# Optimization experiments

Hardware: AMD Instinct MI355X
Metric: run time of the kernel (lower is better)

Reference implementation:

```python
import jax, jax.numpy as jnp
import numpy as np

N, E, IN_DIM, HID = 50000, 800000, 128, 64
NEG_SLOPE = 0.01  # torch F.leaky_relu default


def setup_inputs() -> dict:
    key = jax.random.key(0)
    ks = jax.random.split(key, 8)
    x = jax.random.normal(ks[0], (N, IN_DIM), jnp.float32)
    edge_index = jax.random.randint(ks[1], (2, E), 0, N, dtype=jnp.int32)
    edge_weight = jax.random.uniform(ks[2], (E,), jnp.float32)
    h = jnp.zeros((N, HID), jnp.float32)
    c = jnp.zeros((N, HID), jnp.float32)
    sx = 1.0 / np.sqrt(IN_DIM)
    sh = 1.0 / np.sqrt(HID)
    # gate order along leading axis: [i, f, c(tilde), o]; K=2 Chebyshev weights
    Wx = (jax.random.normal(ks[3], (4, 2, IN_DIM, HID), jnp.float32) * sx)
    bx = jnp.zeros((4, HID), jnp.float32)
    Wh = (jax.random.normal(ks[4], (4, 2, HID, HID), jnp.float32) * sh)
    bh = jnp.zeros((4, HID), jnp.float32)
    wc = jax.random.normal(ks[5], (3, HID), jnp.float32) * 0.1  # peepholes for i, f, o
    bg = jnp.zeros((4, HID), jnp.float32)
    W_head = jax.random.normal(ks[6], (HID, 1), jnp.float32) * sh
    b_head = jnp.zeros((1,), jnp.float32)
    return dict(x=x, edge_index=edge_index, edge_weight=edge_weight, h=h, c=c,
                Wx=Wx, bx=bx, Wh=Wh, bh=bh, wc=wc, bg=bg, W_head=W_head, b_head=b_head)


def _cheb_norm(src, dst, ew, n):
    # ChebConv 'sym' normalization with lambda_max=2: L_hat = -D^{-1/2} A D^{-1/2}
    # (the +1 self-loop from the Laplacian cancels against fill_value=-1)
    deg = jnp.zeros((n,), ew.dtype).at[src].add(ew)
    dinv = jnp.where(deg > 0, 1.0 / jnp.sqrt(jnp.where(deg > 0, deg, 1.0)), 0.0)
    return -dinv[src] * ew * dinv[dst]


def _prop(feat, src, dst, norm, n):
    # T1 = L_hat @ feat via edge gather + segment-sum
    return jax.ops.segment_sum(norm[:, None] * feat[src], dst, num_segments=n)


def reference(x, edge_index, edge_weight, h, c, Wx, bx, Wh, bh, wc, bg, W_head, b_head):
    n = x.shape[0]
    src, dst = edge_index[0], edge_index[1]
    norm = _cheb_norm(src, dst, edge_weight, n)
    Tx = _prop(x, src, dst, norm, n)
    Th = _prop(h, src, dst, norm, n)  # shared across all 4 h-side ChebConvs
    # z[g] = X W[g,0] + (L_hat X) W[g,1] + b  for all gates at once
    z = (jnp.einsum('nd,gdh->gnh', x, Wx[:, 0]) + jnp.einsum('nd,gdh->gnh', Tx, Wx[:, 1]) + bx[:, None, :]
         + jnp.einsum('nd,gdh->gnh', h, Wh[:, 0]) + jnp.einsum('nd,gdh->gnh', Th, Wh[:, 1]) + bh[:, None, :])
    i = jax.nn.sigmoid(z[0] + wc[0] * c + bg[0])
    f = jax.nn.sigmoid(z[1] + wc[1] * c + bg[1])
    g = jnp.tanh(z[2] + bg[2])
    c_new = f * c + i * g
    o = jax.nn.sigmoid(z[3] + wc[2] * c_new + bg[3])
    h_new = o * jnp.tanh(c_new)
    out = jax.nn.leaky_relu(h_new, NEG_SLOPE) @ W_head + b_head
    return out, h_new, c_new
```

## Files before the change

### kernel.cpp

```cpp
#include <hip/hip_runtime.h>
#include <hip/hip_bf16.h>

#define IN_DIM 128
#define HID 64
#define NEG_SLOPE 0.01f
#define CAP 5120

typedef __attribute__((ext_vector_type(8))) short short8;
typedef __attribute__((ext_vector_type(4))) short short4v;
typedef __attribute__((ext_vector_type(4))) float f32x4;
typedef unsigned short ushort_t;
typedef unsigned int uint_t;

__device__ __forceinline__ float fsig(float x) { return 1.f / (1.f + __expf(-x)); }
__device__ __forceinline__ float ftanh(float x) { return 1.f - 2.f / (__expf(2.f * x) + 1.f); }

__device__ __forceinline__ ushort_t f2bf(float f) {
    uint_t u = __float_as_uint(f);
    uint_t r = u + 0x7fffu + ((u >> 16) & 1u);
    return (ushort_t)(r >> 16);
}
__device__ __forceinline__ float bf2f(ushort_t s) { return __uint_as_float(((uint_t)s) << 16); }
__device__ __forceinline__ float bf2f_s(short s) { return bf2f((ushort_t)s); }

__global__ __launch_bounds__(256) void cvt_kernel(
    const float* __restrict__ x, const float* __restrict__ h,
    const float* __restrict__ Wx, const float* __restrict__ Wh,
    uint_t* __restrict__ xb_u, uint_t* __restrict__ hb_u, ushort_t* __restrict__ Wp,
    int N) {
    int tid = blockIdx.x * 256 + threadIdx.x;
    int T = gridDim.x * 256;

    int ncvt = N * 96;
    int nx = N * 64;
    for (int i = tid; i < ncvt; i += T) {
        if (i < nx) {
            float2 v = ((const float2*)x)[i];
            xb_u[i] = (uint_t)f2bf(v.x) | ((uint_t)f2bf(v.y) << 16);
        } else {
            int j = i - nx;
            float2 v = ((const float2*)h)[j];
            hb_u[j] = (uint_t)f2bf(v.x) | ((uint_t)f2bf(v.y) << 16);
        }
    }

    for (int idx = tid; idx < 384 * 256; idx += T) {
        int j = idx & 7;
        int tmp = idx >> 3;
        int lane = tmp & 63;
        int t2 = tmp >> 6;
        int ct = t2 & 15;
        int ks = t2 >> 4;
        int k = ks * 32 + (lane >> 4) * 8 + j;
        int colg = ct * 16 + (lane & 15);
        int g = colg >> 6, hd = colg & 63;
        float v;
        if (k < 128)      v = Wx[((g * 2 + 0) * 128 + k) * 64 + hd];
        else if (k < 192) v = Wh[((g * 2 + 0) * 64 + (k - 128)) * 64 + hd];
        else if (k < 320) v = Wx[((g * 2 + 1) * 128 + (k - 192)) * 64 + hd];
        else              v = Wh[((g * 2 + 1) * 64 + (k - 320)) * 64 + hd];
        Wp[idx] = f2bf(v);
    }
}

__global__ __launch_bounds__(256) void part_kernel(
    const int* __restrict__ src, const int* __restrict__ dst, const float* __restrict__ ew,
    int* __restrict__ cur_d, int* __restrict__ cur_s,
    int2* __restrict__ dpart, int2* __restrict__ spart, int E) {
    __shared__ int hd[256], hs[256];
    int t = threadIdx.x;
    hd[t] = 0; hs[t] = 0;
    __syncthreads();
    int base = blockIdx.x * 2048;
    int sv[8], dv[8]; float wv[8];
#pragma unroll
    for (int it = 0; it < 8; ++it) {
        int e = base + it * 256 + t;
        bool ok = e < E;
        sv[it] = ok ? src[e] : 0;
        dv[it] = ok ? dst[e] : 0;
        wv[it] = ok ? ew[e] : 0.f;
        if (ok) {
            atomicAdd(&hd[dv[it] >> 8], 1);
            atomicAdd(&hs[sv[it] >> 8], 1);
        }
    }
    __syncthreads();
    int nd = hd[t], ns = hs[t];
    __syncthreads();
    if (nd) hd[t] = atomicAdd(&cur_d[t * 16], nd);
    if (ns) hs[t] = atomicAdd(&cur_s[t * 16], ns);
    __syncthreads();
#pragma unroll
    for (int it = 0; it < 8; ++it) {
        int e = base + it * 256 + t;
        if (e < E) {
            int d = dv[it], s = sv[it];
            int bd = d >> 8, bs = s >> 8;
            int pd = atomicAdd(&hd[bd], 1);
            int ps = atomicAdd(&hs[bs], 1);
            dpart[(size_t)bd * CAP + pd] = make_int2(s | ((d & 255) << 16), __float_as_int(wv[it]));
            spart[(size_t)bs * CAP + ps] = make_int2(s & 255, __float_as_int(wv[it]));
        }
    }
}

__global__ __launch_bounds__(256) void deg_kernel(const int2* __restrict__ spart,
                                                  const int* __restrict__ cur_s,
                                                  float* __restrict__ dinv, int N) {
    __shared__ float df[256];
    int t = threadIdx.x, b = blockIdx.x;
    df[t] = 0.f;
    __syncthreads();
    int cnt = cur_s[b * 16];
    for (int i = t; i < cnt; i += 256) {
        int2 r = spart[(size_t)b * CAP + i];
        atomicAdd(&df[r.x & 255], __int_as_float(r.y));
    }
    __syncthreads();
    int g = b * 256 + t;
    if (g < N) {
        float dd = df[t];
        dinv[g] = dd > 0.f ? rsqrtf(dd) : 0.f;
    }
}

__global__ __launch_bounds__(256) void fillb_kernel(const int2* __restrict__ dpart,
                                                    const int* __restrict__ cur_d,
                                                    const float* __restrict__ dinv,
                                                    int* __restrict__ rowptr, int* __restrict__ rowend,
                                                    int2* __restrict__ eprm, int N) {
    __shared__ int c[256], sdata[256], pcur[256];
    __shared__ float dl[256];
    int t = threadIdx.x, b = blockIdx.x;
    c[t] = 0;
    int g = b * 256 + t;
    dl[t] = (g < N) ? dinv[g] : 0.f;
    __syncthreads();
    int cnt = cur_d[b * 16];
    for (int i = t; i < cnt; i += 256) {
        int m = dpart[(size_t)b * CAP + i].x;
        atomicAdd(&c[(m >> 16) & 255], 1);
    }
    __syncthreads();
    sdata[t] = c[t];
    __syncthreads();
    for (int off = 1; off < 256; off <<= 1) {
        int tmp = (t >= off) ? sdata[t - off] : 0;
        __syncthreads();
        sdata[t] += tmp;
        __syncthreads();
    }
    int excl = sdata[t] - c[t];
    pcur[t] = excl;
    if (g < N) {
        rowptr[g] = b * CAP + excl;
        rowend[g] = b * CAP + sdata[t];
    }
    __syncthreads();
    for (int i = t; i < cnt; i += 256) {
        int2 r = dpart[(size_t)b * CAP + i];
        int m = r.x;
        int dlo = (m >> 16) & 255;
        int s = m & 0xffff;
        float w = __int_as_float(r.y);
        int pos = atomicAdd(&pcur[dlo], 1);
        float nrm = -dinv[s] * w * dl[dlo];
        eprm[(size_t)b * CAP + pos] = make_int2(s, __float_as_int(nrm));
    }
}

__global__ __launch_bounds__(256) void gather_kernel(const int* __restrict__ rowptr,
                                                     const int* __restrict__ rowend,
                                                     const int2* __restrict__ eprm,
                                                     const ushort_t* __restrict__ xb,
                                                     const ushort_t* __restrict__ hb,
                                                     ushort_t* __restrict__ Txb,
                                                     ushort_t* __restrict__ Thb, int N) {
    int lane = threadIdx.x & 63;
    int wave = threadIdx.x >> 6;
    int grp = lane >> 4, l16 = lane & 15;
    int node = blockIdx.x * 16 + wave * 4 + grp;
    bool valid = node < N;
    int p = 0, end = 0;
    if (valid) { p = rowptr[node]; end = rowend[node]; }

    float ax[8] = {0.f, 0.f, 0.f, 0.f, 0.f, 0.f, 0.f, 0.f};
    float ah[4] = {0.f, 0.f, 0.f, 0.f};

    int idx0 = p + l16;
    int2 pr = (idx0 < end) ? eprm[idx0] : make_int2(0, 0);

    for (int base = p; base < end; base += 16) {
        int2 cur = pr;
        int nidx = base + 16 + l16;
        if (base + 16 < end) pr = (nidx < end) ? eprm[nidx] : make_int2(0, 0);
        int sv = cur.x;
        float wv = __int_as_float(cur.y);
        int mcount = end - base; if (mcount > 16) mcount = 16;
        int sl0 = grp * 16;
        int j = 0;
        for (; j + 4 <= mcount; j += 4) {
            int s0 = __shfl(sv, sl0 + j + 0), s1 = __shfl(sv, sl0 + j + 1);
            int s2 = __shfl(sv, sl0 + j + 2), s3 = __shfl(sv, sl0 + j + 3);
            float w0 = __shfl(wv, sl0 + j + 0), w1 = __shfl(wv, sl0 + j + 1);
            float w2 = __shfl(wv, sl0 + j + 2), w3 = __shfl(wv, sl0 + j + 3);
            short8 xv0 = *(const short8*)(xb + (size_t)s0 * 128 + l16 * 8);
            short8 xv1 = *(const short8*)(xb + (size_t)s1 * 128 + l16 * 8);
            short8 xv2 = *(const short8*)(xb + (size_t)s2 * 128 + l16 * 8);
            short8 xv3 = *(const short8*)(xb + (size_t)s3 * 128 + l16 * 8);
            short4v hv0 = *(const short4v*)(hb + (size_t)s0 * 64 + l16 * 4);
            short4v hv1 = *(const short4v*)(hb + (size_t)s1 * 64 + l16 * 4);
            short4v hv2 = *(const short4v*)(hb + (size_t)s2 * 64 + l16 * 4);
            short4v hv3 = *(const short4v*)(hb + (size_t)s3 * 64 + l16 * 4);
#pragma unroll
            for (int i = 0; i < 8; ++i)
                ax[i] += w0 * bf2f_s(xv0[i]) + w1 * bf2f_s(xv1[i])
                       + w2 * bf2f_s(xv2[i]) + w3 * bf2f_s(xv3[i]);
#pragma unroll
            for (int i = 0; i < 4; ++i)
                ah[i] += w0 * bf2f_s(hv0[i]) + w1 * bf2f_s(hv1[i])
                       + w2 * bf2f_s(hv2[i]) + w3 * bf2f_s(hv3[i]);
        }
        for (; j < mcount; ++j) {
            int s0 = __shfl(sv, sl0 + j);
            float w0 = __shfl(wv, sl0 + j);
            short8 xv0 = *(const short8*)(xb + (size_t)s0 * 128 + l16 * 8);
            short4v hv0 = *(const short4v*)(hb + (size_t)s0 * 64 + l16 * 4);
#pragma unroll
            for (int i = 0; i < 8; ++i) ax[i] += w0 * bf2f_s(xv0[i]);
#pragma unroll
            for (int i = 0; i < 4; ++i) ah[i] += w0 * bf2f_s(hv0[i]);
        }
    }

    if (valid) {
        short8 tx;
#pragma unroll
        for (int i = 0; i < 8; ++i) tx[i] = (short)f2bf(ax[i]);
        *(short8*)(Txb + (size_t)node * 128 + l16 * 8) = tx;
        short4v th;
#pragma unroll
        for (int i = 0; i < 4; ++i) th[i] = (short)f2bf(ah[i]);
        *(short4v*)(Thb + (size_t)node * 64 + l16 * 4) = th;
    }
}

__global__ __launch_bounds__(256, 4) void fused_mfma(
    const ushort_t* __restrict__ xb, const ushort_t* __restrict__ hb,
    const ushort_t* __restrict__ Txb, const ushort_t* __restrict__ Thb,
    const float* __restrict__ c_in, const ushort_t* __restrict__ Wp,
    const float* __restrict__ bx, const float* __restrict__ bh,
    const float* __restrict__ wc, const float* __restrict__ bg,
    const float* __restrict__ Whead, const float* __restrict__ bhead,
    float* __restrict__ out, int N) {
    __shared__ ushort_t Bs[2][8192];
    int tid = threadIdx.x;
    int lane = tid & 63;
    int wave = tid >> 6;
    int quad = lane >> 4, m = lane & 15;
    int row0 = (blockIdx.x * 4 + wave) * 16;
    int ar = row0 + m; if (ar >= N) ar = N - 1;

    {
        const float4* gsrc = (const float4*)(Wp);
        float4* ldst = (float4*)Bs[0];
#pragma unroll
        for (int i = 0; i < 4; ++i) ldst[tid + 256 * i] = gsrc[tid + 256 * i];
    }

    f32x4 acc[16];
#pragma unroll
    for (int ct = 0; ct < 16; ++ct) {
        int g = ct >> 2, hd = (ct & 3) * 16 + m;
        float b = bx[g * 64 + hd] + bh[g * 64 + hd];
        f32x4 bb = {b, b, b, b};
        acc[ct] = bb;
    }

    int ko = quad * 8;
    __syncthreads();

#pragma unroll
    for (int ks = 0; ks < 12; ++ks) {
        int buf = ks & 1;
        float4 tmp[4];
        if (ks < 11) {
            const float4* gsrc = (const float4*)(Wp + (ks + 1) * 8192);
#pragma unroll
            for (int i = 0; i < 4; ++i) tmp[i] = gsrc[tid + 256 * i];
        }
        const ushort_t* a;
        if (ks < 4)       a = xb  + (size_t)ar * 128 + ks * 32 + ko;
        else if (ks < 6)  a = hb  + (size_t)ar * 64 + (ks - 4) * 32 + ko;
        else if (ks < 10) a = Txb + (size_t)ar * 128 + (ks - 6) * 32 + ko;
        else              a = Thb + (size_t)ar * 64 + (ks - 10) * 32 + ko;
        short8 af = *(const short8*)a;
        const short8* bsp = (const short8*)Bs[buf];
#pragma unroll
        for (int ct = 0; ct < 16; ++ct) {
            short8 bf = bsp[ct * 64 + lane];
            acc[ct] = __builtin_amdgcn_mfma_f32_16x16x32_bf16(af, bf, acc[ct], 0, 0, 0);
        }
        if (ks < 11) {
            float4* ldst = (float4*)Bs[buf ^ 1];
#pragma unroll
            for (int i = 0; i < 4; ++i) ldst[tid + 256 * i] = tmp[i];
            __syncthreads();
        }
    }

    float hp[4] = {0.f, 0.f, 0.f, 0.f};
    float bhv = bhead[0];

#pragma unroll
    for (int hs = 0; hs < 4; ++hs) {
        int hd = hs * 16 + m;
        float wc0 = wc[hd], wc1 = wc[64 + hd], wc2 = wc[128 + hd];
        float bg0 = bg[hd], bg1 = bg[64 + hd], bg2 = bg[128 + hd], bg3 = bg[192 + hd];
        float wh = Whead[hd];
#pragma unroll
        for (int reg = 0; reg < 4; ++reg) {
            int n = row0 + quad * 4 + reg;
            if (n < N) {
                float c_old = c_in[(size_t)n * 64 + hd];
                float zi = acc[0 * 4 + hs][reg];
                float zf = acc[1 * 4 + hs][reg];
                float zg = acc[2 * 4 + hs][reg];
                float zo = acc[3 * 4 + hs][reg];
                float ii = fsig(zi + wc0 * c_old + bg0);
                float ff = fsig(zf + wc1 * c_old + bg1);
                float gg = ftanh(zg + bg2);
                float cn = ff * c_old + ii * gg;
                float oo = fsig(zo + wc2 * cn + bg3);
                float hn = oo * ftanh(cn);
                out[N + (size_t)n * 64 + hd] = hn;
                out[N + (size_t)N * 64 + (size_t)n * 64 + hd] = cn;
                float lr = hn > 0.f ? hn : NEG_SLOPE * hn;
                hp[reg] += lr * wh;
            }
        }
    }
#pragma unroll
    for (int reg = 0; reg < 4; ++reg) {
        float v0 = hp[reg];
#pragma unroll
        for (int mask = 1; mask < 16; mask <<= 1) v0 += __shfl_xor(v0, mask);
        if (m == 0) {
            int n0_ = row0 + quad * 4 + reg;
            if (n0_ < N) out[n0_] = v0 + bhv;
        }
    }
}

extern "C" void kernel_launch(void* const* d_in, const int* in_sizes, int n_in,
                              void* d_out, int out_size, void* d_ws, size_t ws_size,
                              hipStream_t stream) {
    const float* x = (const float*)d_in[0];
    const int* ei = (const int*)d_in[1];
    const float* ew = (const float*)d_in[2];
    const float* h = (const float*)d_in[3];
    const float* c = (const float*)d_in[4];
    const float* Wx = (const float*)d_in[5];
    const float* bx = (const float*)d_in[6];
    const float* Wh = (const float*)d_in[7];
    const float* bh = (const float*)d_in[8];
    const float* wc = (const float*)d_in[9];
    const float* bg = (const float*)d_in[10];
    const float* Whead = (const float*)d_in[11];
    const float* bhead = (const float*)d_in[12];

    int N = in_sizes[0] / IN_DIM;
    int E = in_sizes[1] / 2;
    const int* src = ei;
    const int* dst = ei + E;

    int nbuck = (N + 255) >> 8;

    char* wp = (char*)d_ws;
    auto alloc = [&](size_t bytes) {
        char* p = wp;
        wp += (bytes + 255) & ~(size_t)255;
        return p;
    };
    int* cur = (int*)alloc((size_t)2 * nbuck * 16 * 4);
    int* cur_d = cur;
    int* cur_s = cur + (size_t)nbuck * 16;
    float* dinv = (float*)alloc((size_t)N * 4);
    int* rowptr = (int*)alloc((size_t)N * 4);
    int* rowend = (int*)alloc((size_t)N * 4);
    int2* dpart = (int2*)alloc((size_t)nbuck * CAP * 8);
    int2* spart = (int2*)alloc((size_t)nbuck * CAP * 8);
    int2* eprm = spart;
    ushort_t* xb = (ushort_t*)alloc((size_t)N * 128 * 2);
    ushort_t* hb = (ushort_t*)alloc((size_t)N * 64 * 2);
    ushort_t* Txb = (ushort_t*)alloc((size_t)N * 128 * 2);
    ushort_t* Thb = (ushort_t*)alloc((size_t)N * 64 * 2);
    ushort_t* Wp = (ushort_t*)alloc((size_t)384 * 256 * 2);

    hipMemsetAsync(cur, 0, (size_t)2 * nbuck * 16 * 4, stream);

    part_kernel<<<(E + 2047) / 2048, 256, 0, stream>>>(src, dst, ew, cur_d, cur_s,
                                                       dpart, spart, E);
    cvt_kernel<<<2048, 256, 0, stream>>>(x, h, Wx, Wh, (uint_t*)xb, (uint_t*)hb, Wp, N);
    deg_kernel<<<nbuck, 256, 0, stream>>>(spart, cur_s, dinv, N);
    fillb_kernel<<<nbuck, 256, 0, stream>>>(dpart, cur_d, dinv, rowptr, rowend, eprm, N);
    gather_kernel<<<(N + 15) / 16, 256, 0, stream>>>(rowptr, rowend, eprm, xb, hb, Txb, Thb, N);
    fused_mfma<<<(N + 63) / 64, 256, 0, stream>>>(xb, hb, Txb, Thb, c, Wp, bx, bh, wc, bg,
                                                  Whead, bhead, (float*)d_out, N);
}
```

Measured before the change: 239.4 us.

## Fuse bf16 conversion into partition kernel, widen gather unroll, preload A fragments

Merges the cvt kernel into the edge partition kernel so both run in one launch with a grid of about 391 blocks, which saves a launch and lets the conversion overlap with the partitioning. The gather loop now processes 8 neighbours per step instead of 4, putting more independent loads in flight. The MFMA kernel loads all 12 A fragments into registers before the K loop, taking the global loads off the per-step critical path. The cost is higher register pressure, which may reduce occupancy, and a smaller grid for the conversion work.

```diff
diff --git a/kernel.cpp b/kernel.cpp
--- a/kernel.cpp
+++ b/kernel.cpp
@@ -23,14 +23,53 @@
 __device__ __forceinline__ float bf2f(ushort_t s) { return __uint_as_float(((uint_t)s) << 16); }
 __device__ __forceinline__ float bf2f_s(short s) { return bf2f((ushort_t)s); }
 
-__global__ __launch_bounds__(256) void cvt_kernel(
+__global__ __launch_bounds__(256) void part_kernel(
+    const int* __restrict__ src, const int* __restrict__ dst, const float* __restrict__ ew,
     const float* __restrict__ x, const float* __restrict__ h,
     const float* __restrict__ Wx, const float* __restrict__ Wh,
+    int* __restrict__ cur_d, int* __restrict__ cur_s,
+    int2* __restrict__ dpart, int2* __restrict__ spart,
     uint_t* __restrict__ xb_u, uint_t* __restrict__ hb_u, ushort_t* __restrict__ Wp,
-    int N) {
-    int tid = blockIdx.x * 256 + threadIdx.x;
+    int E, int N) {
+    __shared__ int hd[256], hs[256];
+    int t = threadIdx.x;
+    hd[t] = 0; hs[t] = 0;
+    __syncthreads();
+    int base = blockIdx.x * 2048;
+    int sv[8], dv[8]; float wv[8];
+#pragma unroll
+    for (int it = 0; it < 8; ++it) {
+        int e = base + it * 256 + t;
+        bool ok = e < E;
+        sv[it] = ok ? src[e] : 0;
+        dv[it] = ok ? dst[e] : 0;
+        wv[it] = ok ? ew[e] : 0.f;
+        if (ok) {
+            atomicAdd(&hd[dv[it] >> 8], 1);
+            atomicAdd(&hs[sv[it] >> 8], 1);
+        }
+    }
+    __syncthreads();
+    int nd = hd[t], ns = hs[t];
+    __syncthreads();
+    if (nd) hd[t] = atomicAdd(&cur_d[t * 16], nd);
+    if (ns) hs[t] = atomicAdd(&cur_s[t * 16], ns);
+    __syncthreads();
+#pragma unroll
+    for (int it = 0; it < 8; ++it) {
+        int e = base + it * 256 + t;
+        if (e < E) {
+            int d = dv[it], s = sv[it];
+            int bd = d >> 8, bs = s >> 8;
+            int pd = atomicAdd(&hd[bd], 1);
+            int ps = atomicAdd(&hs[bs], 1);
+            dpart[(size_t)bd * CAP + pd] = make_int2(s | ((d & 255) << 16), __float_as_int(wv[it]));
+            spart[(size_t)bs * CAP + ps] = make_int2(s & 255, __float_as_int(wv[it]));
+        }
+    }
+
+    int tid = blockIdx.x * 256 + t;
     int T = gridDim.x * 256;
-
     int ncvt = N * 96;
     int nx = N * 64;
     for (int i = tid; i < ncvt; i += T) {
@@ -53,55 +92,13 @@
         int ks = t2 >> 4;
         int k = ks * 32 + (lane >> 4) * 8 + j;
         int colg = ct * 16 + (lane & 15);
-        int g = colg >> 6, hd = colg & 63;
+        int g = colg >> 6, hdd = colg & 63;
         float v;
-        if (k < 128)      v = Wx[((g * 2 + 0) * 128 + k) * 64 + hd];
-        else if (k < 192) v = Wh[((g * 2 + 0) * 64 + (k - 128)) * 64 + hd];
-        else if (k < 320) v = Wx[((g * 2 + 1) * 128 + (k - 192)) * 64 + hd];
-        else              v = Wh[((g * 2 + 1) * 64 + (k - 320)) * 64 + hd];
+        if (k < 128)      v = Wx[((g * 2 + 0) * 128 + k) * 64 + hdd];
+        else if (k < 192) v = Wh[((g * 2 + 0) * 64 + (k - 128)) * 64 + hdd];
+        else if (k < 320) v = Wx[((g * 2 + 1) * 128 + (k - 192)) * 64 + hdd];
+        else              v = Wh[((g * 2 + 1) * 64 + (k - 320)) * 64 + hdd];
         Wp[idx] = f2bf(v);
-    }
-}
-
-__global__ __launch_bounds__(256) void part_kernel(
-    const int* __restrict__ src, const int* __restrict__ dst, const float* __restrict__ ew,
-    int* __restrict__ cur_d, int* __restrict__ cur_s,
-    int2* __restrict__ dpart, int2* __restrict__ spart, int E) {
-    __shared__ int hd[256], hs[256];
-    int t = threadIdx.x;
-    hd[t] = 0; hs[t] = 0;
-    __syncthreads();
-    int base = blockIdx.x * 2048;
-    int sv[8], dv[8]; float wv[8];
-#pragma unroll
-    for (int it = 0; it < 8; ++it) {
-        int e = base + it * 256 + t;
-        bool ok = e < E;
-        sv[it] = ok ? src[e] : 0;
-        dv[it] = ok ? dst[e] : 0;
-        wv[it] = ok ? ew[e] : 0.f;
-        if (ok) {
-            atomicAdd(&hd[dv[it] >> 8], 1);
-            atomicAdd(&hs[sv[it] >> 8], 1);
-        }
-    }
-    __syncthreads();
-    int nd = hd[t], ns = hs[t];
-    __syncthreads();
-    if (nd) hd[t] = atomicAdd(&cur_d[t * 16], nd);
-    if (ns) hs[t] = atomicAdd(&cur_s[t * 16], ns);
-    __syncthreads();
-#pragma unroll
-    for (int it = 0; it < 8; ++it) {
-        int e = base + it * 256 + t;
-        if (e < E) {
-            int d = dv[it], s = sv[it];
-            int bd = d >> 8, bs = s >> 8;
-            int pd = atomicAdd(&hd[bd], 1);
-            int ps = atomicAdd(&hs[bs], 1);
-            dpart[(size_t)bd * CAP + pd] = make_int2(s | ((d & 255) << 16), __float_as_int(wv[it]));
-            spart[(size_t)bs * CAP + ps] = make_int2(s & 255, __float_as_int(wv[it]));
-        }
     }
 }
 
@@ -200,27 +197,26 @@
         int mcount = end - base; if (mcount > 16) mcount = 16;
         int sl0 = grp * 16;
         int j = 0;
-        for (; j + 4 <= mcount; j += 4) {
-            int s0 = __shfl(sv, sl0 + j + 0), s1 = __shfl(sv, sl0 + j + 1);
-            int s2 = __shfl(sv, sl0 + j + 2), s3 = __shfl(sv, sl0 + j + 3);
-            float w0 = __shfl(wv, sl0 + j + 0), w1 = __shfl(wv, sl0 + j + 1);
-            float w2 = __shfl(wv, sl0 + j + 2), w3 = __shfl(wv, sl0 + j + 3);
-            short8 xv0 = *(const short8*)(xb + (size_t)s0 * 128 + l16 * 8);
-            short8 xv1 = *(const short8*)(xb + (size_t)s1 * 128 + l16 * 8);
-            short8 xv2 = *(const short8*)(xb + (size_t)s2 * 128 + l16 * 8);
-            short8 xv3 = *(const short8*)(xb + (size_t)s3 * 128 + l16 * 8);
-            short4v hv0 = *(const short4v*)(hb + (size_t)s0 * 64 + l16 * 4);
-            short4v hv1 = *(const short4v*)(hb + (size_t)s1 * 64 + l16 * 4);
-            short4v hv2 = *(const short4v*)(hb + (size_t)s2 * 64 + l16 * 4);
-            short4v hv3 = *(const short4v*)(hb + (size_t)s3 * 64 + l16 * 4);
-#pragma unroll
-            for (int i = 0; i < 8; ++i)
-                ax[i] += w0 * bf2f_s(xv0[i]) + w1 * bf2f_s(xv1[i])
-                       + w2 * bf2f_s(xv2[i]) + w3 * bf2f_s(xv3[i]);
-#pragma unroll
-            for (int i = 0; i < 4; ++i)
-                ah[i] += w0 * bf2f_s(hv0[i]) + w1 * bf2f_s(hv1[i])
-                       + w2 * bf2f_s(hv2[i]) + w3 * bf2f_s(hv3[i]);
+        for (; j + 8 <= mcount; j += 8) {
+            int s_[8]; float w_[8];
+#pragma unroll
+            for (int q = 0; q < 8; ++q) {
+                s_[q] = __shfl(sv, sl0 + j + q);
+                w_[q] = __shfl(wv, sl0 + j + q);
+            }
+            short8 xv[8]; short4v hv[8];
+#pragma unroll
+            for (int q = 0; q < 8; ++q) {
+                xv[q] = *(const short8*)(xb + (size_t)s_[q] * 128 + l16 * 8);
+                hv[q] = *(const short4v*)(hb + (size_t)s_[q] * 64 + l16 * 4);
+            }
+#pragma unroll
+            for (int q = 0; q < 8; ++q) {
+#pragma unroll
+                for (int i = 0; i < 8; ++i) ax[i] += w_[q] * bf2f_s(xv[q][i]);
+#pragma unroll
+                for (int i = 0; i < 4; ++i) ah[i] += w_[q] * bf2f_s(hv[q][i]);
+            }
         }
         for (; j < mcount; ++j) {
             int s0 = __shfl(sv, sl0 + j);
@@ -261,6 +257,18 @@
     int quad = lane >> 4, m = lane & 15;
     int row0 = (blockIdx.x * 4 + wave) * 16;
     int ar = row0 + m; if (ar >= N) ar = N - 1;
+    int ko = quad * 8;
+
+    short8 afr[12];
+#pragma unroll
+    for (int ks = 0; ks < 12; ++ks) {
+        const ushort_t* a;
+        if (ks < 4)       a = xb  + (size_t)ar * 128 + ks * 32 + ko;
+        else if (ks < 6)  a = hb  + (size_t)ar * 64 + (ks - 4) * 32 + ko;
+        else if (ks < 10) a = Txb + (size_t)ar * 128 + (ks - 6) * 32 + ko;
+        else              a = Thb + (size_t)ar * 64 + (ks - 10) * 32 + ko;
+        afr[ks] = *(const short8*)a;
+    }
 
     {
         const float4* gsrc = (const float4*)(Wp);
@@ -278,7 +286,6 @@
         acc[ct] = bb;
     }
 
-    int ko = quad * 8;
     __syncthreads();
 
 #pragma unroll
@@ -290,17 +297,11 @@
 #pragma unroll
             for (int i = 0; i < 4; ++i) tmp[i] = gsrc[tid + 256 * i];
         }
-        const ushort_t* a;
-        if (ks < 4)       a = xb  + (size_t)ar * 128 + ks * 32 + ko;
-        else if (ks < 6)  a = hb  + (size_t)ar * 64 + (ks - 4) * 32 + ko;
-        else if (ks < 10) a = Txb + (size_t)ar * 128 + (ks - 6) * 32 + ko;
-        else              a = Thb + (size_t)ar * 64 + (ks - 10) * 32 + ko;
-        short8 af = *(const short8*)a;
         const short8* bsp = (const short8*)Bs[buf];
 #pragma unroll
         for (int ct = 0; ct < 16; ++ct) {
             short8 bf = bsp[ct * 64 + lane];
-            acc[ct] = __builtin_amdgcn_mfma_f32_16x16x32_bf16(af, bf, acc[ct], 0, 0, 0);
+            acc[ct] = __builtin_amdgcn_mfma_f32_16x16x32_bf16(afr[ks], bf, acc[ct], 0, 0, 0);
         }
         if (ks < 11) {
             float4* ldst = (float4*)Bs[buf ^ 1];
@@ -400,9 +401,9 @@
 
     hipMemsetAsync(cur, 0, (size_t)2 * nbuck * 16 * 4, stream);
 
-    part_kernel<<<(E + 2047) / 2048, 256, 0, stream>>>(src, dst, ew, cur_d, cur_s,
-                                                       dpart, spart, E);
-    cvt_kernel<<<2048, 256, 0, stream>>>(x, h, Wx, Wh, (uint_t*)xb, (uint_t*)hb, Wp, N);
+    part_kernel<<<(E + 2047) / 2048, 256, 0, stream>>>(src, dst, ew, x, h, Wx, Wh,
+                                                       cur_d, cur_s, dpart, spart,
+                                                       (uint_t*)xb, (uint_t*)hb, Wp, E, N);
     deg_kernel<<<nbuck, 256, 0, stream>>>(spart, cur_s, dinv, N);
     fillb_kernel<<<nbuck, 256, 0, stream>>>(dpart, cur_d, dinv, rowptr, rowend, eprm, N);
     gather_kernel<<<(N + 15) / 16, 256, 0, stream>>>(rowptr, rowend, eprm, xb, hb, Txb, Thb, N);
```

Measured after the change: 278.4 us. 1.16x slower.
